# Performance work log

Measured on AMD Instinct MI355X. Metric: run time of the kernel, lower is better.

The kernel has to match this reference:

```python
import jax, jax.numpy as jnp
import numpy as np

PI = 3.1415926
NPERSEG, HOP = 512, 256
NFRAMES = 17
NFFT_BINS = 257
S = NFFT_BINS * NFRAMES  # 4369
NPATCH = 196
NFREQ = NPATCH // 2 + 1  # 99
D = 128
NF = 2
B = 32
TLEN = 4096

# periodic hann window (scipy default for spectral analysis)
_win_np = (0.5 - 0.5 * np.cos(2.0 * np.pi * np.arange(NPERSEG) / NPERSEG)).astype(np.float32)
WIN = jnp.asarray(_win_np)
WSUM = float(_win_np.sum())  # = 256
_idx_np = np.arange(NFRAMES)[:, None] * HOP + np.arange(NPERSEG)[None, :]
IDX = jnp.asarray(_idx_np)
IDX_FLAT = jnp.asarray(_idx_np.reshape(-1))
OLA_LEN = NPERSEG + (NFRAMES - 1) * HOP  # 4608


def _stft(x):
    # x: (B, D, T) real -> (B, D, 257, 17) complex; matches scipy.signal.stft
    # (window='hann', nperseg=512, noverlap=256, boundary='zeros', 'spectrum' scaling)
    xp = jnp.pad(x, ((0, 0), (0, 0), (HOP, HOP)))
    segs = xp[:, :, IDX] * WIN  # (B, D, 17, 512)
    Z = jnp.fft.rfft(segs, axis=-1) / WSUM
    return jnp.swapaxes(Z, -1, -2)


def _istft(Z):
    # Z: (B, D, 257, 17) complex -> (B, D, 4096) real; matches scipy.signal.istft
    b, d = Z.shape[0], Z.shape[1]
    frames = jnp.fft.irfft(Z, n=NPERSEG, axis=2) * WSUM * WIN[:, None]  # (B, D, 512, 17)
    frames = jnp.swapaxes(frames, 2, 3).reshape(b, d, NFRAMES * NPERSEG)
    ola = jnp.zeros((b, d, OLA_LEN), frames.dtype).at[:, :, IDX_FLAT].add(frames)
    norm = jnp.zeros((OLA_LEN,), frames.dtype).at[IDX_FLAT].add(jnp.tile(WIN * WIN, NFRAMES))
    return (ola / jnp.where(norm > 1e-10, norm, 1.0))[:, :, HOP:-HOP]


def _cx(p):
    return p[..., 0] + 1j * p[..., 1]


def _filter_bank(x, length, fb):
    # x * x / length summed against filter bank with dct-like cosine coefficients
    c = jnp.cos((2.0 * jnp.arange(1, NF + 1, dtype=jnp.float32) - 1.0) * PI / 2.0 * NF)
    fb_eff = jnp.sum(_cx(fb) * c[:, None, None], axis=0)
    return (x * x / length) * fb_eff


def _ln(x, g, b):
    m = x.mean(-1, keepdims=True)
    v = ((x - m) ** 2).mean(-1, keepdims=True)
    return (x - m) / jnp.sqrt(v + 1e-5) * g + b


def _addnorm(x, g1, b1, w1, bb1, w2, bb2, g2, b2):
    x = _ln(x, g1, b1)
    h = jax.nn.gelu(x @ w1 + bb1, approximate=False) @ w2 + bb2 + x
    return _ln(h, g2, b2)


def setup_inputs():
    key = jax.random.key(0)
    ks = jax.random.split(key, 12)
    sc = 0.05
    d = {}
    d["ecg"] = jax.random.normal(ks[0], (B, TLEN, D), jnp.float32)
    d["image"] = jax.random.normal(ks[1], (B, NPATCH, D), jnp.float32)
    d["tfb"] = jax.random.normal(ks[2], (NF, S, D, 2), jnp.float32)
    d["ifb"] = jax.random.normal(ks[3], (NF, NFREQ, D, 2), jnp.float32)
    d["i2t_sel"] = jax.random.normal(ks[4], (NFREQ, D, 2), jnp.float32)
    d["i2t_w"] = jax.random.normal(ks[5], (D, D), jnp.float32) * sc
    d["i2t_b"] = jnp.zeros((D,), jnp.float32)
    d["t_ln1_g"] = jnp.ones((D,), jnp.float32)
    d["t_ln1_b"] = jnp.zeros((D,), jnp.float32)
    d["t_w1"] = jax.random.normal(ks[6], (D, D), jnp.float32) * sc
    d["t_b1"] = jnp.zeros((D,), jnp.float32)
    d["t_w2"] = jax.random.normal(ks[7], (D, D), jnp.float32) * sc
    d["t_b2"] = jnp.zeros((D,), jnp.float32)
    d["t_ln2_g"] = jnp.ones((D,), jnp.float32)
    d["t_ln2_b"] = jnp.zeros((D,), jnp.float32)
    d["i_ln1_g"] = jnp.ones((D,), jnp.float32)
    d["i_ln1_b"] = jnp.zeros((D,), jnp.float32)
    d["i_w1"] = jax.random.normal(ks[8], (D, D), jnp.float32) * sc
    d["i_b1"] = jnp.zeros((D,), jnp.float32)
    d["i_w2"] = jax.random.normal(ks[9], (D, D), jnp.float32) * sc
    d["i_b2"] = jnp.zeros((D,), jnp.float32)
    d["i_ln2_g"] = jnp.ones((D,), jnp.float32)
    d["i_ln2_b"] = jnp.zeros((D,), jnp.float32)
    return d


def reference(ecg, image, tfb, ifb, i2t_sel, i2t_w, i2t_b,
              t_ln1_g, t_ln1_b, t_w1, t_b1, t_w2, t_b2, t_ln2_g, t_ln2_b,
              i_ln1_g, i_ln1_b, i_w1, i_b1, i_w2, i_b2, i_ln2_g, i_ln2_b):
    b, tlen, dm = ecg.shape
    n = image.shape[1]
    Z = _stft(jnp.swapaxes(ecg, 1, 2))  # (B, D, 257, 17)
    z_ecg = jnp.transpose(Z, (0, 2, 3, 1)).reshape(b, S, dm)  # (B, 4369, D) complex
    z_ecg = _filter_bank(z_ecg, S, tfb)
    z_img = jnp.fft.rfft(image, axis=1, norm="ortho")  # (B, 99, D)
    z_img = _filter_bank(z_img, NFREQ, ifb)
    # Image2TextGate: complex select, avg-pool real part over freq bins, 1x1 conv
    g = (z_img * _cx(i2t_sel)).real.mean(axis=1)  # (B, D)
    gate = (jnp.einsum("bd,ed->be", g, i2t_w) + i2t_b)[:, None, :]  # (B, 1, D)
    z_sel = z_ecg * gate
    ecg_t = _istft(jnp.transpose(z_sel.reshape(b, NFFT_BINS, NFRAMES, dm), (0, 3, 1, 2)))
    # torch detaches via numpy roundtrip -> stop_gradient
    ecg_t = jax.lax.stop_gradient(jnp.swapaxes(ecg_t, 1, 2))  # (B, T, D)
    text = _addnorm(ecg_t + ecg, t_ln1_g, t_ln1_b, t_w1, t_b1, t_w2, t_b2, t_ln2_g, t_ln2_b)
    # NOTE: original code discards image_frequency_select output and irffts the
    # filtered _image directly (bug preserved faithfully).
    img_t = jnp.fft.irfft(z_img, n=n, axis=1, norm="ortho")
    img_out = _addnorm(img_t + image, i_ln1_g, i_ln1_b, i_w1, i_b1, i_w2, i_b2, i_ln2_g, i_ln2_b)
    return (text, img_out)
```

## Files before the change

kernel.cpp:

```cpp
#include <hip/hip_runtime.h>
#include <math.h>

#define BB 32
#define DD 128
#define TLEN 4096
#define NSEG 512
#define HOP 256
#define NFR 17
#define NBINS 257
#define STOT 4369
#define NPATCH 196
#define NFREQ 99
#define OLAL 4608

#define FBT2_OFF 0
#define FBT2_SZ  (DD * NFR * NBINS * 2)
#define GBUF_OFF (FBT2_OFF + FBT2_SZ)
#define GATE_OFF (GBUF_OFF + BB * DD)
#define ZI_OFF   (GATE_OFF + BB * DD)
#define ZI_SZ    (BB * NFREQ * DD * 2)
#define X0I_OFF  (ZI_OFF + ZI_SZ)
#define X0I_SZ   (BB * NPATCH * DD)
#define XT_OFF   (X0I_OFF + X0I_SZ)
#define WF_OFF   (XT_OFF + BB * DD * TLEN)

typedef __attribute__((ext_vector_type(8))) short bf16x8;
typedef __attribute__((ext_vector_type(4))) float f32x4;
typedef __attribute__((ext_vector_type(8))) unsigned short u16x8;

__device__ __forceinline__ float gelu_exact(float x) {
    return 0.5f * x * (1.0f + erff(x * 0.70710678118654752f));
}

__device__ __forceinline__ short bf16_rne(float v) {
    unsigned b = __float_as_uint(v);
    return (short)((b + 0x7fffu + ((b >> 16) & 1u)) >> 16);
}

__device__ __forceinline__ void split8(float4 a, float4 b, bf16x8& hi, bf16x8& lo) {
    float v[8] = {a.x, a.y, a.z, a.w, b.x, b.y, b.z, b.w};
#pragma unroll
    for (int e = 0; e < 8; ++e) {
        unsigned bv = __float_as_uint(v[e]);
        unsigned hb = (bv + 0x7fffu + ((bv >> 16) & 1u)) & 0xffff0000u;
        float hf = __uint_as_float(hb);
        hi[e] = (short)(hb >> 16);
        lo[e] = bf16_rne(v[e] - hf);
    }
}

__global__ __launch_bounds__(256) void prep_wfrag(
    const float* __restrict__ w0, const float* __restrict__ w1,
    const float* __restrict__ w2, const float* __restrict__ w3,
    unsigned short* __restrict__ outw) {
    int id = blockIdx.x * 256 + threadIdx.x;
    if (id >= 4 * 2048) return;
    int m = id >> 11;
    int r = id & 2047;
    int kt = r >> 9;
    int n = (r >> 6) & 7;
    int lane = r & 63;
    int k0 = kt * 32 + (lane >> 4) * 8;
    int col = n * 16 + (lane & 15);
    const float* w = (m == 0) ? w0 : (m == 1) ? w1 : (m == 2) ? w2 : w3;
    u16x8 hi, lo;
#pragma unroll
    for (int e = 0; e < 8; ++e) {
        float v = w[(size_t)(k0 + e) * DD + col];
        unsigned bv = __float_as_uint(v);
        unsigned hb = (bv + 0x7fffu + ((bv >> 16) & 1u)) & 0xffff0000u;
        float hf = __uint_as_float(hb);
        float lres = v - hf;
        unsigned bl = __float_as_uint(lres);
        hi[e] = (unsigned short)(hb >> 16);
        lo[e] = (unsigned short)((bl + 0x7fffu + ((bl >> 16) & 1u)) >> 16);
    }
    u16x8* base = (u16x8*)(outw + (size_t)m * 32768);
    base[r] = hi;
    base[2048 + r] = lo;
}

__global__ __launch_bounds__(256) void prep_fb(const float* __restrict__ tfb,
                                               float* __restrict__ fbt2,
                                               float* __restrict__ gbuf) {
    int idx = blockIdx.x * 256 + threadIdx.x;
    if (idx < BB * DD) gbuf[idx] = 0.0f;
    if (idx >= STOT * DD) return;
    int d = idx & 127;
    int s = idx >> 7;
    float2 a = ((const float2*)tfb)[s * DD + d];
    float2 b = ((const float2*)tfb)[STOT * DD + s * DD + d];
    int f = s / NFR, t = s % NFR;
    float2 r;
    r.x = -(a.x + b.x);
    r.y = -(a.y + b.y);
    ((float2*)fbt2)[((size_t)d * NFR + t) * NBINS + f] = r;
}

__global__ __launch_bounds__(256) void transpose_btd(const float* __restrict__ in,
                                                     float* __restrict__ out) {
    __shared__ float tile[32][33];
    int b = blockIdx.z;
    int t0 = blockIdx.x * 32;
    int d0 = blockIdx.y * 32;
    int lx = threadIdx.x;
    int ly = threadIdx.y;
    for (int i = ly; i < 32; i += 8)
        tile[i][lx] = in[((size_t)b * TLEN + t0 + i) * DD + d0 + lx];
    __syncthreads();
    for (int i = ly; i < 32; i += 8)
        out[((size_t)b * DD + d0 + i) * TLEN + t0 + lx] = tile[lx][i];
}

__global__ __launch_bounds__(128) void img_dft(const float* __restrict__ image,
                                               const float* __restrict__ ifb,
                                               const float* __restrict__ sel,
                                               float* __restrict__ zi,
                                               float* __restrict__ gbuf) {
    __shared__ float ctab[NPATCH], stab[NPATCH];
    int b = blockIdx.x / 11;
    int fg = blockIdx.x % 11;
    int d = threadIdx.x;
    for (int m = d; m < NPATCH; m += 128) {
        ctab[m] = cospif(m * (2.0f / 196.0f));
        stab[m] = sinpif(m * (2.0f / 196.0f));
    }
    __syncthreads();
    float accr[9], acci[9];
    int mc[9];
#pragma unroll
    for (int j = 0; j < 9; ++j) { accr[j] = 0.0f; acci[j] = 0.0f; mc[j] = 0; }
    const float* img = image + (size_t)b * NPATCH * DD + d;
    for (int n = 0; n < NPATCH; ++n) {
        float v = img[(size_t)n * DD];
#pragma unroll
        for (int j = 0; j < 9; ++j) {
            float c = ctab[mc[j]], s = stab[mc[j]];
            accr[j] += v * c;
            acci[j] -= v * s;
            mc[j] += fg * 9 + j;
            if (mc[j] >= NPATCH) mc[j] -= NPATCH;
        }
    }
    float gg = 0.0f;
#pragma unroll
    for (int j = 0; j < 9; ++j) {
        int f = fg * 9 + j;
        float Xr = accr[j] * (1.0f / 14.0f);
        float Xi = acci[j] * (1.0f / 14.0f);
        float sr = (Xr * Xr - Xi * Xi) * (1.0f / 99.0f);
        float si = 2.0f * Xr * Xi * (1.0f / 99.0f);
        float2 f0 = ((const float2*)ifb)[f * DD + d];
        float2 f1 = ((const float2*)ifb)[NFREQ * DD + f * DD + d];
        float fbr = -(f0.x + f1.x), fbi = -(f0.y + f1.y);
        float zr = sr * fbr - si * fbi;
        float zm = sr * fbi + si * fbr;
        float2 o; o.x = zr; o.y = zm;
        ((float2*)zi)[((size_t)b * NFREQ + f) * DD + d] = o;
        float2 sl = ((const float2*)sel)[f * DD + d];
        gg += zr * sl.x - zm * sl.y;
    }
    atomicAdd(gbuf + b * DD + d, gg * (1.0f / 99.0f));
}

__global__ __launch_bounds__(128) void gate_kernel(const float* __restrict__ gbuf,
                                                   const float* __restrict__ w,
                                                   const float* __restrict__ bias,
                                                   float* __restrict__ gate) {
    __shared__ float gs[DD];
    int b = blockIdx.x, e = threadIdx.x;
    gs[e] = gbuf[b * DD + e];
    __syncthreads();
    float acc = bias[e];
    const float* wr = w + (size_t)e * DD;
    for (int d = 0; d < DD; ++d) acc += gs[d] * wr[d];
    gate[b * DD + e] = acc;
}

#define SWZ(e) ((e) ^ (((e) >> 4) & 15))

#define CMULW(dr, di, c, s, xr, xi) { float _t = (dr)*(c) - (di)*(s); xi = (dr)*(s) + (di)*(c); xr = _t; }
#define BF(xr, xi, h) { \
    float pr_ = __shfl_xor(xr, h), pi_ = __shfl_xor(xi, h); \
    float dr2_ = fmaf(sg##h, xr, pr_), di2_ = fmaf(sg##h, xi, pi_); \
    CMULW(dr2_, di2_, tc##h, ts##h, xr, xi) }
#define SSTG(h) BF(a0r, a0i, h) BF(a1r, a1i, h) BF(a2r, a2i, h) BF(a3r, a3i, h)
#define BF1(xr, xi) { \
    float pr_ = __shfl_xor(xr, 1), pi_ = __shfl_xor(xi, 1); \
    xr = fmaf(sg1, xr, pr_); xi = fmaf(sg1, xi, pi_); }
#define DIF256() { \
    float dr_, di_; \
    dr_ = a0r - a2r; di_ = a0i - a2i; a0r += a2r; a0i += a2i; CMULW(dr_, di_, wa_c, wa_s, a2r, a2i) \
    dr_ = a1r - a3r; di_ = a1i - a3i; a1r += a3r; a1i += a3i; CMULW(dr_, di_, wb_c, wb_s, a3r, a3i) \
    dr_ = a0r - a1r; di_ = a0i - a1i; a0r += a1r; a0i += a1i; CMULW(dr_, di_, wc_c, wc_s, a1r, a1i) \
    dr_ = a2r - a3r; di_ = a2i - a3i; a2r += a3r; a2i += a3i; CMULW(dr_, di_, wc_c, wc_s, a3r, a3i) \
    SSTG(32) SSTG(16) SSTG(8) SSTG(4) SSTG(2) \
    BF1(a0r, a0i) BF1(a1r, a1i) BF1(a2r, a2i) BF1(a3r, a3i) }

__global__ __launch_bounds__(256, 4) void stft_filter_istft(
    float* xT, const float* __restrict__ fbt2, const float* __restrict__ gate) {
    __shared__ float2 spec[NFR * 256];
    __shared__ float win[NSEG];
    __shared__ float rnorm[256];
    __shared__ float mct[129], mst[129];
    int tid = threadIdx.x;
    int lane = tid & 63, wave = tid >> 6;
    int bd = blockIdx.x;
    int d = bd & 127;
    float gat = gate[bd];
    const float scl = gat * (1.0f / 4369.0f);
    float* xrow = xT + (size_t)bd * TLEN;
    const float2* fbrow = (const float2*)(fbt2 + (size_t)d * NFR * NBINS * 2);

    for (int j = tid; j < NSEG; j += 256)
        win[j] = 0.5f - 0.5f * cospif(j * (1.0f / 256.0f));
    {
        float s2 = 0.5f - 0.5f * cospif(tid * (1.0f / 256.0f));
        float c2 = 1.0f - s2;
        rnorm[tid] = 1.0f / (s2 * s2 + c2 * c2);
    }
    if (tid < 129) {
        mct[tid] = cospif(tid * (1.0f / 256.0f));
        mst[tid] = sinpif(tid * (1.0f / 256.0f));
    }

    float wa_c = cospif(lane * (1.0f / 128.0f)), wa_s = -sinpif(lane * (1.0f / 128.0f));
    float wb_c = cospif((64 + lane) * (1.0f / 128.0f)), wb_s = -sinpif((64 + lane) * (1.0f / 128.0f));
    float wc_c = cospif(lane * (1.0f / 64.0f)),  wc_s = -sinpif(lane * (1.0f / 64.0f));
#define MKT(h) \
    float tc##h, ts##h, sg##h; \
    { int set_ = lane & h; float ang_ = (float)(lane & (h - 1)) * (1.0f / h); \
      tc##h = set_ ? cospif(ang_) : 1.0f; \
      ts##h = set_ ? -sinpif(ang_) : 0.0f; \
      sg##h = set_ ? -1.0f : 1.0f; }
    MKT(32) MKT(16) MKT(8) MKT(4) MKT(2)
    float sg1 = (lane & 1) ? -1.0f : 1.0f;
#undef MKT

    int eS[4], eL[4];
#pragma unroll
    for (int j = 0; j < 4; ++j) {
        int i = j * 64 + lane;
        eS[j] = SWZ((int)(__brev((unsigned)i) >> 24));
        eL[j] = SWZ(i);
    }
    __syncthreads();

    for (int t = wave; t < NFR; t += 4) {
        float a0r, a0i, a1r, a1i, a2r, a2i, a3r, a3i;
#define LOADJ(j, xr, xi) { \
        int i_ = (j) * 64 + lane; \
        int src_ = t * HOP + 2 * i_ - HOP; \
        float er_ = 0.0f, oi_ = 0.0f; \
        if (src_ >= 0 && src_ < TLEN) { \
            float2 v_ = *(const float2*)(xrow + src_); er_ = v_.x; oi_ = v_.y; } \
        float2 w_ = *(const float2*)(win + 2 * i_); \
        xr = er_ * w_.x; xi = oi_ * w_.y; }
        LOADJ(0, a0r, a0i) LOADJ(1, a1r, a1i) LOADJ(2, a2r, a2i) LOADJ(3, a3r, a3i)
#undef LOADJ
        DIF256()
        float2* sp = spec + t * 256;
        sp[eS[0]] = make_float2(a0r, a0i);
        sp[eS[1]] = make_float2(a1r, a1i);
        sp[eS[2]] = make_float2(a2r, a2i);
        sp[eS[3]] = make_float2(a3r, a3i);
    }
    __syncthreads();

    for (int j = tid; j < NFR * 129; j += 256) {
        int t = j / 129, m = j - t * 129;
        float2* sp = spec + t * 256;
        const float2* fbr = fbrow + t * NBINS;
        if (m == 0) {
            float2 v = sp[0];
            float re = v.x, im = v.y;
            float z0 = (re + im) * (1.0f / 256.0f);
            float zN = (re - im) * (1.0f / 256.0f);
            float2 fb0 = fbr[0], fbN = fbr[256];
            float y1r = z0 * z0 * fb0.x * scl;
            float y2r = zN * zN * fbN.x * scl;
            float Er = 0.5f * (y1r + y2r);
            float Dr = 0.5f * (y1r - y2r);
            sp[0] = make_float2(Er, -Dr);
        } else if (m == 128) {
            float2 v = sp[SWZ(128)];
            float Zr = v.x, Zi = v.y;
            float zr = Zr * (1.0f / 256.0f), zi2 = -Zi * (1.0f / 256.0f);
            float sr = zr * zr - zi2 * zi2, si = 2.0f * zr * zi2;
            float2 fb = fbr[128];
            sp[SWZ(128)] = make_float2((sr * fb.x - si * fb.y) * scl,
                                       (sr * fb.y + si * fb.x) * scl);
        } else {
            float2 vm = sp[SWZ(m)];
            float2 vc = sp[SWZ(256 - m)];
            float Amr = vm.x, Ami = vm.y;
            float Acr = vc.x, Aci = vc.y;
            float c = mct[m];
            float sn = mst[m];
            float y1r, y1i, y2r, y2i;
            {
                float Br = Acr, Bi = -Aci;
                float xer = 0.5f * (Amr + Br), xei = 0.5f * (Ami + Bi);
                float xo_r = 0.5f * (Ami - Bi), xo_i = -0.5f * (Amr - Br);
                float Xr = xer + c * xo_r + sn * xo_i;
                float Xi = xei + c * xo_i - sn * xo_r;
                float zr = Xr * (1.0f / 256.0f), zi2 = Xi * (1.0f / 256.0f);
                float sr = zr * zr - zi2 * zi2, si = 2.0f * zr * zi2;
                float2 fb = fbr[m];
                y1r = (sr * fb.x - si * fb.y) * scl;
                y1i = (sr * fb.y + si * fb.x) * scl;
            }
            {
                float Br = Amr, Bi = -Ami;
                float xer = 0.5f * (Acr + Br), xei = 0.5f * (Aci + Bi);
                float xo_r = 0.5f * (Aci - Bi), xo_i = -0.5f * (Acr - Br);
                float Xr = xer - c * xo_r + sn * xo_i;
                float Xi = xei - c * xo_i - sn * xo_r;
                float zr = Xr * (1.0f / 256.0f), zi2 = Xi * (1.0f / 256.0f);
                float sr = zr * zr - zi2 * zi2, si = 2.0f * zr * zi2;
                float2 fb = fbr[256 - m];
                y2r = (sr * fb.x - si * fb.y) * scl;
                y2i = (sr * fb.y + si * fb.x) * scl;
            }
            float Er = 0.5f * (y1r + y2r);
            float Ei = 0.5f * (y1i - y2i);
            float Dr = 0.5f * (y1r - y2r);
            float Di = 0.5f * (y1i + y2i);
            float Or = Dr * c - Di * sn;
            float Oi = Dr * sn + Di * c;
            sp[SWZ(m)] = make_float2(Er - Oi, -(Ei + Or));
            sp[SWZ(256 - m)] = make_float2(Er + Oi, Ei - Or);
        }
    }
    __syncthreads();

    for (int t = wave; t < NFR; t += 4) {
        float2* sp = spec + t * 256;
        float2 v0 = sp[eL[0]], v1 = sp[eL[1]], v2 = sp[eL[2]], v3 = sp[eL[3]];
        float a0r = v0.x, a0i = v0.y, a1r = v1.x, a1i = v1.y;
        float a2r = v2.x, a2i = v2.y, a3r = v3.x, a3i = v3.y;
        DIF256()
        sp[eS[0]] = make_float2(a0r, a0i);
        sp[eS[1]] = make_float2(a1r, a1i);
        sp[eS[2]] = make_float2(a2r, a2i);
        sp[eS[3]] = make_float2(a3r, a3i);
    }
    __syncthreads();

    const float* specf = (const float*)spec;
    for (int j = tid; j < TLEN; j += 256) {
        int p = j + HOP;
        int t1 = p >> 8, t0 = t1 - 1;
        int i1 = p & 255, i0 = i1 + 256;
        int comp = j & 1;
        float v1 = specf[(t1 * 256 + SWZ(i1 >> 1)) * 2 + comp];
        float v0 = specf[(t0 * 256 + SWZ(i0 >> 1)) * 2 + comp];
        if (comp) { v1 = -v1; v0 = -v0; }
        float s = v0 * win[i0] + v1 * win[i1];
        xrow[j] = s * rnorm[i1];
    }
}

__global__ __launch_bounds__(128) void img_irfft(const float* __restrict__ zi,
                                                 const float* __restrict__ image,
                                                 float* __restrict__ x0img) {
    __shared__ float ctab[NPATCH], stab[NPATCH];
    int b = blockIdx.x / 14;
    int ng = blockIdx.x % 14;
    int d = threadIdx.x;
    for (int m = d; m < NPATCH; m += 128) {
        ctab[m] = cospif(m * (2.0f / 196.0f));
        stab[m] = sinpif(m * (2.0f / 196.0f));
    }
    __syncthreads();
    const float2* zrow = (const float2*)zi + (size_t)b * NFREQ * DD + d;
    float acc[14];
    int mc[14];
    float2 z0 = zrow[0];
#pragma unroll
    for (int j = 0; j < 14; ++j) { acc[j] = z0.x; mc[j] = 0; }
    for (int f = 1; f <= 97; ++f) {
        float2 z = zrow[(size_t)f * DD];
#pragma unroll
        for (int j = 0; j < 14; ++j) {
            int n = ng * 14 + j;
            mc[j] += n;
            if (mc[j] >= NPATCH) mc[j] -= NPATCH;
            acc[j] += 2.0f * (z.x * ctab[mc[j]] - z.y * stab[mc[j]]);
        }
    }
    float2 z98 = zrow[98 * (size_t)DD];
#pragma unroll
    for (int j = 0; j < 14; ++j) {
        int n = ng * 14 + j;
        float a = acc[j] + ((n & 1) ? -z98.x : z98.x);
        float y = a * (1.0f / 14.0f);
        size_t idx = ((size_t)b * NPATCH + n) * DD + d;
        x0img[idx] = y + image[idx];
    }
}

#define XLNS 132

__device__ __forceinline__ void mlp_gemm(const float* __restrict__ ax,
                                         const unsigned short* __restrict__ wf,
                                         int lane, f32x4 acc[8]) {
#pragma unroll
    for (int n = 0; n < 8; ++n) acc[n] = (f32x4){0.f, 0.f, 0.f, 0.f};
    const bf16x8* bh0 = (const bf16x8*)wf;
    const bf16x8* bl0 = (const bf16x8*)(wf + 16384);
#pragma unroll 1
    for (int kt = 0; kt < 4; ++kt) {
        float4 va = *(const float4*)(ax + kt * 32);
        float4 vb = *(const float4*)(ax + kt * 32 + 4);
        bf16x8 ahi, alo;
        split8(va, vb, ahi, alo);
        const bf16x8* bh = bh0 + kt * 512 + lane;
        const bf16x8* bl = bl0 + kt * 512 + lane;
#pragma unroll
        for (int n = 0; n < 8; ++n) {
            bf16x8 wh = bh[n * 64];
            bf16x8 wl = bl[n * 64];
            acc[n] = __builtin_amdgcn_mfma_f32_16x16x32_bf16(ahi, wh, acc[n], 0, 0, 0);
            acc[n] = __builtin_amdgcn_mfma_f32_16x16x32_bf16(alo, wh, acc[n], 0, 0, 0);
            acc[n] = __builtin_amdgcn_mfma_f32_16x16x32_bf16(ahi, wl, acc[n], 0, 0, 0);
        }
    }
}

template <int FUSED>
__global__ __launch_bounds__(256) void addnorm_kernel(
    const float* __restrict__ srcA, const float* __restrict__ srcB,
    const float* __restrict__ ln1g, const float* __restrict__ ln1b,
    const unsigned short* __restrict__ w1f, const float* __restrict__ b1,
    const unsigned short* __restrict__ w2f, const float* __restrict__ b2,
    const float* __restrict__ ln2g, const float* __restrict__ ln2b,
    float* __restrict__ out) {
    __shared__ __align__(16) float xln[64 * XLNS];
    int tid = threadIdx.x;
    int b = 0, t0 = 0;
    size_t R0 = 0;
    if (FUSED) {
        b = blockIdx.x >> 6;
        t0 = (blockIdx.x & 63) * 64;
        for (int i = tid; i < 64 * 128; i += 256) {
            int dd = i >> 6, r = i & 63;
            xln[r * XLNS + dd] = srcA[((size_t)b * DD + dd) * TLEN + t0 + r];
        }
        __syncthreads();
        for (int i = tid; i < 64 * 128; i += 256) {
            int r = i >> 7, dd = i & 127;
            xln[r * XLNS + dd] += srcB[((size_t)b * TLEN + t0 + r) * DD + dd];
        }
    } else {
        R0 = (size_t)blockIdx.x * 64;
        for (int i = tid; i < 64 * 128; i += 256) {
            int r = i >> 7, dd = i & 127;
            xln[r * XLNS + dd] = srcA[(R0 + r) * DD + dd];
        }
    }
    __syncthreads();
    int wave = tid >> 6, lane = tid & 63;
    for (int r = wave; r < 64; r += 4) {
        float v0 = xln[r * XLNS + lane];
        float v1 = xln[r * XLNS + 64 + lane];
        float s = v0 + v1, ss = v0 * v0 + v1 * v1;
        for (int off = 32; off > 0; off >>= 1) {
            s += __shfl_xor(s, off);
            ss += __shfl_xor(ss, off);
        }
        float mean = s * (1.0f / 128.0f);
        float var = ss * (1.0f / 128.0f) - mean * mean;
        float rstd = rsqrtf(var + 1e-5f);
        xln[r * XLNS + lane] = (v0 - mean) * rstd * ln1g[lane] + ln1b[lane];
        xln[r * XLNS + 64 + lane] = (v1 - mean) * rstd * ln1g[64 + lane] + ln1b[64 + lane];
    }
    __syncthreads();
    int q = lane >> 4, c = lane & 15;
    int rbase = wave * 16 + q * 4;
    const float* ax = &xln[(wave * 16 + c) * XLNS + q * 8];
    f32x4 acc[8];
    mlp_gemm(ax, w1f, lane, acc);
    float res[8][4];
#pragma unroll
    for (int n = 0; n < 8; ++n)
#pragma unroll
        for (int r = 0; r < 4; ++r)
            res[n][r] = xln[(rbase + r) * XLNS + n * 16 + c];
#pragma unroll
    for (int n = 0; n < 8; ++n) {
        float bb = b1[n * 16 + c];
#pragma unroll
        for (int r = 0; r < 4; ++r)
            acc[n][r] = gelu_exact(acc[n][r] + bb);
    }
    __syncthreads();
#pragma unroll
    for (int n = 0; n < 8; ++n)
#pragma unroll
        for (int r = 0; r < 4; ++r)
            xln[(rbase + r) * XLNS + n * 16 + c] = acc[n][r];
    __syncthreads();
    mlp_gemm(ax, w2f, lane, acc);
#pragma unroll
    for (int n = 0; n < 8; ++n) {
        float bb = b2[n * 16 + c];
#pragma unroll
        for (int r = 0; r < 4; ++r)
            acc[n][r] += bb + res[n][r];
    }
    float s4[4] = {0.f, 0.f, 0.f, 0.f}, ss4[4] = {0.f, 0.f, 0.f, 0.f};
#pragma unroll
    for (int n = 0; n < 8; ++n)
#pragma unroll
        for (int r = 0; r < 4; ++r) {
            float h = acc[n][r];
            s4[r] += h; ss4[r] += h * h;
        }
#pragma unroll
    for (int off = 8; off > 0; off >>= 1) {
#pragma unroll
        for (int r = 0; r < 4; ++r) {
            s4[r] += __shfl_xor(s4[r], off);
            ss4[r] += __shfl_xor(ss4[r], off);
        }
    }
    float g2v[8], b2v[8];
#pragma unroll
    for (int n = 0; n < 8; ++n) {
        g2v[n] = ln2g[n * 16 + c];
        b2v[n] = ln2b[n * 16 + c];
    }
#pragma unroll
    for (int r = 0; r < 4; ++r) {
        float mean = s4[r] * (1.0f / 128.0f);
        float var = ss4[r] * (1.0f / 128.0f) - mean * mean;
        float rstd = rsqrtf(var + 1e-5f);
        size_t orow = FUSED ? ((size_t)b * TLEN + t0 + rbase + r) * DD
                            : (R0 + rbase + r) * DD;
#pragma unroll
        for (int n = 0; n < 8; ++n)
            out[orow + n * 16 + c] = (acc[n][r] - mean) * rstd * g2v[n] + b2v[n];
    }
}

extern "C" void kernel_launch(void* const* d_in, const int* in_sizes, int n_in,
                              void* d_out, int out_size, void* d_ws, size_t ws_size,
                              hipStream_t stream) {
    (void)in_sizes; (void)n_in; (void)out_size; (void)ws_size;
    const float* ecg   = (const float*)d_in[0];
    const float* image = (const float*)d_in[1];
    const float* tfb   = (const float*)d_in[2];
    const float* ifb   = (const float*)d_in[3];
    const float* sel   = (const float*)d_in[4];
    const float* i2t_w = (const float*)d_in[5];
    const float* i2t_b = (const float*)d_in[6];
    const float* t_ln1_g = (const float*)d_in[7];
    const float* t_ln1_b = (const float*)d_in[8];
    const float* t_w1 = (const float*)d_in[9];
    const float* t_b1 = (const float*)d_in[10];
    const float* t_w2 = (const float*)d_in[11];
    const float* t_b2 = (const float*)d_in[12];
    const float* t_ln2_g = (const float*)d_in[13];
    const float* t_ln2_b = (const float*)d_in[14];
    const float* i_ln1_g = (const float*)d_in[15];
    const float* i_ln1_b = (const float*)d_in[16];
    const float* i_w1 = (const float*)d_in[17];
    const float* i_b1 = (const float*)d_in[18];
    const float* i_w2 = (const float*)d_in[19];
    const float* i_b2 = (const float*)d_in[20];
    const float* i_ln2_g = (const float*)d_in[21];
    const float* i_ln2_b = (const float*)d_in[22];
    float* out = (float*)d_out;
    float* ws = (float*)d_ws;
    unsigned short* wfb = (unsigned short*)(ws + WF_OFF);

    prep_wfrag<<<32, 256, 0, stream>>>(t_w1, t_w2, i_w1, i_w2, wfb);
    prep_fb<<<(STOT * DD + 255) / 256, 256, 0, stream>>>(tfb, ws + FBT2_OFF, ws + GBUF_OFF);
    {
        dim3 tb(32, 8);
        dim3 tg(TLEN / 32, DD / 32, BB);
        transpose_btd<<<tg, tb, 0, stream>>>(ecg, ws + XT_OFF);
    }
    img_dft<<<BB * 11, 128, 0, stream>>>(image, ifb, sel, ws + ZI_OFF, ws + GBUF_OFF);
    gate_kernel<<<BB, 128, 0, stream>>>(ws + GBUF_OFF, i2t_w, i2t_b, ws + GATE_OFF);
    stft_filter_istft<<<BB * DD, 256, 0, stream>>>(ws + XT_OFF, ws + FBT2_OFF, ws + GATE_OFF);
    addnorm_kernel<1><<<BB * (TLEN / 64), 256, 0, stream>>>(
        ws + XT_OFF, ecg, t_ln1_g, t_ln1_b, wfb + 0, t_b1, wfb + 32768, t_b2,
        t_ln2_g, t_ln2_b, out);
    img_irfft<<<BB * 14, 128, 0, stream>>>(ws + ZI_OFF, image, ws + X0I_OFF);
    addnorm_kernel<0><<<(BB * NPATCH) / 64, 256, 0, stream>>>(
        ws + X0I_OFF, nullptr, i_ln1_g, i_ln1_b, wfb + 65536, i_b1, wfb + 98304, i_b2,
        i_ln2_g, i_ln2_b, out + (size_t)BB * TLEN * DD);
}
```

Measured before the change: 591.2 us.

## Merge prep kernels and overlap image irfft with text addnorm launch

Combines the weight-fragment prep, filter-bank transpose, ECG transpose and image DFT into one block-range-dispatched kernel. The image irfft is folded into the same launch as the text add-norm. The image gate reduction now writes per-group partial sums that gate_kernel adds up, replacing the atomics and the buffer zeroing. In the text add-norm, the residual ECG add moves into the LayerNorm pass, removing one shared-memory pass and a barrier. The aim is fewer launches and less tail idle time, at the cost of heterogeneous blocks sharing one launch configuration.

```diff
diff --git a/kernel.cpp b/kernel.cpp
--- a/kernel.cpp
+++ b/kernel.cpp
@@ -49,127 +49,144 @@
     }
 }
 
-__global__ __launch_bounds__(256) void prep_wfrag(
-    const float* __restrict__ w0, const float* __restrict__ w1,
-    const float* __restrict__ w2, const float* __restrict__ w3,
-    unsigned short* __restrict__ outw) {
-    int id = blockIdx.x * 256 + threadIdx.x;
-    if (id >= 4 * 2048) return;
-    int m = id >> 11;
-    int r = id & 2047;
-    int kt = r >> 9;
-    int n = (r >> 6) & 7;
-    int lane = r & 63;
-    int k0 = kt * 32 + (lane >> 4) * 8;
-    int col = n * 16 + (lane & 15);
-    const float* w = (m == 0) ? w0 : (m == 1) ? w1 : (m == 2) ? w2 : w3;
-    u16x8 hi, lo;
-#pragma unroll
-    for (int e = 0; e < 8; ++e) {
-        float v = w[(size_t)(k0 + e) * DD + col];
-        unsigned bv = __float_as_uint(v);
-        unsigned hb = (bv + 0x7fffu + ((bv >> 16) & 1u)) & 0xffff0000u;
-        float hf = __uint_as_float(hb);
-        float lres = v - hf;
-        unsigned bl = __float_as_uint(lres);
-        hi[e] = (unsigned short)(hb >> 16);
-        lo[e] = (unsigned short)((bl + 0x7fffu + ((bl >> 16) & 1u)) >> 16);
-    }
-    u16x8* base = (u16x8*)(outw + (size_t)m * 32768);
-    base[r] = hi;
-    base[2048 + r] = lo;
-}
-
-__global__ __launch_bounds__(256) void prep_fb(const float* __restrict__ tfb,
-                                               float* __restrict__ fbt2,
-                                               float* __restrict__ gbuf) {
-    int idx = blockIdx.x * 256 + threadIdx.x;
-    if (idx < BB * DD) gbuf[idx] = 0.0f;
-    if (idx >= STOT * DD) return;
-    int d = idx & 127;
-    int s = idx >> 7;
-    float2 a = ((const float2*)tfb)[s * DD + d];
-    float2 b = ((const float2*)tfb)[STOT * DD + s * DD + d];
-    int f = s / NFR, t = s % NFR;
-    float2 r;
-    r.x = -(a.x + b.x);
-    r.y = -(a.y + b.y);
-    ((float2*)fbt2)[((size_t)d * NFR + t) * NBINS + f] = r;
-}
-
-__global__ __launch_bounds__(256) void transpose_btd(const float* __restrict__ in,
-                                                     float* __restrict__ out) {
-    __shared__ float tile[32][33];
-    int b = blockIdx.z;
-    int t0 = blockIdx.x * 32;
-    int d0 = blockIdx.y * 32;
-    int lx = threadIdx.x;
-    int ly = threadIdx.y;
-    for (int i = ly; i < 32; i += 8)
-        tile[i][lx] = in[((size_t)b * TLEN + t0 + i) * DD + d0 + lx];
-    __syncthreads();
-    for (int i = ly; i < 32; i += 8)
-        out[((size_t)b * DD + d0 + i) * TLEN + t0 + lx] = tile[lx][i];
-}
-
-__global__ __launch_bounds__(128) void img_dft(const float* __restrict__ image,
-                                               const float* __restrict__ ifb,
-                                               const float* __restrict__ sel,
-                                               float* __restrict__ zi,
-                                               float* __restrict__ gbuf) {
-    __shared__ float ctab[NPATCH], stab[NPATCH];
-    int b = blockIdx.x / 11;
-    int fg = blockIdx.x % 11;
-    int d = threadIdx.x;
-    for (int m = d; m < NPATCH; m += 128) {
-        ctab[m] = cospif(m * (2.0f / 196.0f));
-        stab[m] = sinpif(m * (2.0f / 196.0f));
-    }
-    __syncthreads();
-    float accr[9], acci[9];
-    int mc[9];
-#pragma unroll
-    for (int j = 0; j < 9; ++j) { accr[j] = 0.0f; acci[j] = 0.0f; mc[j] = 0; }
-    const float* img = image + (size_t)b * NPATCH * DD + d;
-    for (int n = 0; n < NPATCH; ++n) {
-        float v = img[(size_t)n * DD];
-#pragma unroll
-        for (int j = 0; j < 9; ++j) {
-            float c = ctab[mc[j]], s = stab[mc[j]];
-            accr[j] += v * c;
-            acci[j] -= v * s;
-            mc[j] += fg * 9 + j;
-            if (mc[j] >= NPATCH) mc[j] -= NPATCH;
-        }
-    }
-    float gg = 0.0f;
-#pragma unroll
-    for (int j = 0; j < 9; ++j) {
-        int f = fg * 9 + j;
-        float Xr = accr[j] * (1.0f / 14.0f);
-        float Xi = acci[j] * (1.0f / 14.0f);
-        float sr = (Xr * Xr - Xi * Xi) * (1.0f / 99.0f);
-        float si = 2.0f * Xr * Xi * (1.0f / 99.0f);
-        float2 f0 = ((const float2*)ifb)[f * DD + d];
-        float2 f1 = ((const float2*)ifb)[NFREQ * DD + f * DD + d];
-        float fbr = -(f0.x + f1.x), fbi = -(f0.y + f1.y);
-        float zr = sr * fbr - si * fbi;
-        float zm = sr * fbi + si * fbr;
-        float2 o; o.x = zr; o.y = zm;
-        ((float2*)zi)[((size_t)b * NFREQ + f) * DD + d] = o;
-        float2 sl = ((const float2*)sel)[f * DD + d];
-        gg += zr * sl.x - zm * sl.y;
-    }
-    atomicAdd(gbuf + b * DD + d, gg * (1.0f / 99.0f));
-}
-
-__global__ __launch_bounds__(128) void gate_kernel(const float* __restrict__ gbuf,
+#define PA_DFT0   0
+#define PA_DFTN   (BB * 11)
+#define PA_WF0    (PA_DFT0 + PA_DFTN)
+#define PA_WFN    32
+#define PA_FB0    (PA_WF0 + PA_WFN)
+#define PA_FBN    ((STOT * DD + 255) / 256)
+#define PA_TR0    (PA_FB0 + PA_FBN)
+#define PA_TRN    ((TLEN / 32) * (DD / 32) * BB)
+#define PA_TOT    (PA_TR0 + PA_TRN)
+
+__global__ __launch_bounds__(256) void prep_all(
+    const float* __restrict__ tw1, const float* __restrict__ tw2,
+    const float* __restrict__ iw1, const float* __restrict__ iw2,
+    unsigned short* __restrict__ outw,
+    const float* __restrict__ tfb, float* __restrict__ fbt2,
+    const float* __restrict__ ecg, float* __restrict__ xT,
+    const float* __restrict__ image, const float* __restrict__ ifb,
+    const float* __restrict__ sel, float* __restrict__ zi,
+    float* __restrict__ gpart) {
+    __shared__ float smem[32 * 33];
+    int bid = blockIdx.x;
+    int tid = threadIdx.x;
+
+    if (bid < PA_DFTN) {
+        float* ctab = smem;
+        float* stab = smem + 200;
+        int b = bid / 11;
+        int fg = bid % 11;
+        for (int m = tid; m < NPATCH; m += 256) {
+            ctab[m] = cospif(m * (2.0f / 196.0f));
+            stab[m] = sinpif(m * (2.0f / 196.0f));
+        }
+        __syncthreads();
+        if (tid < 128) {
+            int d = tid;
+            float accr[9], acci[9];
+            int mc[9];
+#pragma unroll
+            for (int j = 0; j < 9; ++j) { accr[j] = 0.0f; acci[j] = 0.0f; mc[j] = 0; }
+            const float* img = image + (size_t)b * NPATCH * DD + d;
+            for (int n = 0; n < NPATCH; ++n) {
+                float v = img[(size_t)n * DD];
+#pragma unroll
+                for (int j = 0; j < 9; ++j) {
+                    float c = ctab[mc[j]], s = stab[mc[j]];
+                    accr[j] += v * c;
+                    acci[j] -= v * s;
+                    mc[j] += fg * 9 + j;
+                    if (mc[j] >= NPATCH) mc[j] -= NPATCH;
+                }
+            }
+            float gg = 0.0f;
+#pragma unroll
+            for (int j = 0; j < 9; ++j) {
+                int f = fg * 9 + j;
+                float Xr = accr[j] * (1.0f / 14.0f);
+                float Xi = acci[j] * (1.0f / 14.0f);
+                float sr = (Xr * Xr - Xi * Xi) * (1.0f / 99.0f);
+                float si = 2.0f * Xr * Xi * (1.0f / 99.0f);
+                float2 f0 = ((const float2*)ifb)[f * DD + d];
+                float2 f1 = ((const float2*)ifb)[NFREQ * DD + f * DD + d];
+                float fbr = -(f0.x + f1.x), fbi = -(f0.y + f1.y);
+                float zr = sr * fbr - si * fbi;
+                float zm = sr * fbi + si * fbr;
+                float2 o; o.x = zr; o.y = zm;
+                ((float2*)zi)[((size_t)b * NFREQ + f) * DD + d] = o;
+                float2 sl = ((const float2*)sel)[f * DD + d];
+                gg += zr * sl.x - zm * sl.y;
+            }
+            gpart[((size_t)fg * BB + b) * DD + d] = gg * (1.0f / 99.0f);
+        }
+    } else if (bid < PA_FB0) {
+        int id = (bid - PA_WF0) * 256 + tid;
+        if (id < 4 * 2048) {
+            int m = id >> 11;
+            int r = id & 2047;
+            int kt = r >> 9;
+            int n = (r >> 6) & 7;
+            int lane = r & 63;
+            int k0 = kt * 32 + (lane >> 4) * 8;
+            int col = n * 16 + (lane & 15);
+            const float* w = (m == 0) ? tw1 : (m == 1) ? tw2 : (m == 2) ? iw1 : iw2;
+            u16x8 hi, lo;
+#pragma unroll
+            for (int e = 0; e < 8; ++e) {
+                float v = w[(size_t)(k0 + e) * DD + col];
+                unsigned bv = __float_as_uint(v);
+                unsigned hb = (bv + 0x7fffu + ((bv >> 16) & 1u)) & 0xffff0000u;
+                float hf = __uint_as_float(hb);
+                float lres = v - hf;
+                unsigned bl = __float_as_uint(lres);
+                hi[e] = (unsigned short)(hb >> 16);
+                lo[e] = (unsigned short)((bl + 0x7fffu + ((bl >> 16) & 1u)) >> 16);
+            }
+            u16x8* base = (u16x8*)(outw + (size_t)m * 32768);
+            base[r] = hi;
+            base[2048 + r] = lo;
+        }
+    } else if (bid < PA_TR0) {
+        int idx = (bid - PA_FB0) * 256 + tid;
+        if (idx < STOT * DD) {
+            int d = idx & 127;
+            int s = idx >> 7;
+            float2 a = ((const float2*)tfb)[s * DD + d];
+            float2 b2 = ((const float2*)tfb)[STOT * DD + s * DD + d];
+            int f = s / NFR, t = s % NFR;
+            float2 r;
+            r.x = -(a.x + b2.x);
+            r.y = -(a.y + b2.y);
+            ((float2*)fbt2)[((size_t)d * NFR + t) * NBINS + f] = r;
+        }
+    } else {
+        int rel = bid - PA_TR0;
+        int t0 = (rel & 127) * 32;
+        int d0 = ((rel >> 7) & 3) * 32;
+        int b = rel >> 9;
+        int lx = tid & 31;
+        int ly = tid >> 5;
+        float (*tile)[33] = (float (*)[33])smem;
+        for (int i = ly; i < 32; i += 8)
+            tile[i][lx] = ecg[((size_t)b * TLEN + t0 + i) * DD + d0 + lx];
+        __syncthreads();
+        for (int i = ly; i < 32; i += 8)
+            xT[((size_t)b * DD + d0 + i) * TLEN + t0 + lx] = tile[lx][i];
+    }
+}
+
+__global__ __launch_bounds__(128) void gate_kernel(const float* __restrict__ gpart,
                                                    const float* __restrict__ w,
                                                    const float* __restrict__ bias,
                                                    float* __restrict__ gate) {
     __shared__ float gs[DD];
     int b = blockIdx.x, e = threadIdx.x;
-    gs[e] = gbuf[b * DD + e];
+    float acc0 = 0.0f;
+#pragma unroll
+    for (int fg = 0; fg < 11; ++fg)
+        acc0 += gpart[((size_t)fg * BB + b) * DD + e];
+    gs[e] = acc0;
     __syncthreads();
     float acc = bias[e];
     const float* wr = w + (size_t)e * DD;
@@ -361,45 +378,6 @@
     }
 }
 
-__global__ __launch_bounds__(128) void img_irfft(const float* __restrict__ zi,
-                                                 const float* __restrict__ image,
-                                                 float* __restrict__ x0img) {
-    __shared__ float ctab[NPATCH], stab[NPATCH];
-    int b = blockIdx.x / 14;
-    int ng = blockIdx.x % 14;
-    int d = threadIdx.x;
-    for (int m = d; m < NPATCH; m += 128) {
-        ctab[m] = cospif(m * (2.0f / 196.0f));
-        stab[m] = sinpif(m * (2.0f / 196.0f));
-    }
-    __syncthreads();
-    const float2* zrow = (const float2*)zi + (size_t)b * NFREQ * DD + d;
-    float acc[14];
-    int mc[14];
-    float2 z0 = zrow[0];
-#pragma unroll
-    for (int j = 0; j < 14; ++j) { acc[j] = z0.x; mc[j] = 0; }
-    for (int f = 1; f <= 97; ++f) {
-        float2 z = zrow[(size_t)f * DD];
-#pragma unroll
-        for (int j = 0; j < 14; ++j) {
-            int n = ng * 14 + j;
-            mc[j] += n;
-            if (mc[j] >= NPATCH) mc[j] -= NPATCH;
-            acc[j] += 2.0f * (z.x * ctab[mc[j]] - z.y * stab[mc[j]]);
-        }
-    }
-    float2 z98 = zrow[98 * (size_t)DD];
-#pragma unroll
-    for (int j = 0; j < 14; ++j) {
-        int n = ng * 14 + j;
-        float a = acc[j] + ((n & 1) ? -z98.x : z98.x);
-        float y = a * (1.0f / 14.0f);
-        size_t idx = ((size_t)b * NPATCH + n) * DD + d;
-        x0img[idx] = y + image[idx];
-    }
-}
-
 #define XLNS 132
 
 __device__ __forceinline__ void mlp_gemm(const float* __restrict__ ax,
@@ -429,31 +407,26 @@
 }
 
 template <int FUSED>
-__global__ __launch_bounds__(256) void addnorm_kernel(
+__device__ __forceinline__ void addnorm_body(
+    int bid, float* xln,
     const float* __restrict__ srcA, const float* __restrict__ srcB,
     const float* __restrict__ ln1g, const float* __restrict__ ln1b,
     const unsigned short* __restrict__ w1f, const float* __restrict__ b1,
     const unsigned short* __restrict__ w2f, const float* __restrict__ b2,
     const float* __restrict__ ln2g, const float* __restrict__ ln2b,
     float* __restrict__ out) {
-    __shared__ __align__(16) float xln[64 * XLNS];
     int tid = threadIdx.x;
     int b = 0, t0 = 0;
     size_t R0 = 0;
     if (FUSED) {
-        b = blockIdx.x >> 6;
-        t0 = (blockIdx.x & 63) * 64;
+        b = bid >> 6;
+        t0 = (bid & 63) * 64;
         for (int i = tid; i < 64 * 128; i += 256) {
             int dd = i >> 6, r = i & 63;
             xln[r * XLNS + dd] = srcA[((size_t)b * DD + dd) * TLEN + t0 + r];
         }
-        __syncthreads();
-        for (int i = tid; i < 64 * 128; i += 256) {
-            int r = i >> 7, dd = i & 127;
-            xln[r * XLNS + dd] += srcB[((size_t)b * TLEN + t0 + r) * DD + dd];
-        }
     } else {
-        R0 = (size_t)blockIdx.x * 64;
+        R0 = (size_t)bid * 64;
         for (int i = tid; i < 64 * 128; i += 256) {
             int r = i >> 7, dd = i & 127;
             xln[r * XLNS + dd] = srcA[(R0 + r) * DD + dd];
@@ -461,9 +434,14 @@
     }
     __syncthreads();
     int wave = tid >> 6, lane = tid & 63;
+    const float* pB = FUSED ? srcB + ((size_t)b * TLEN + t0) * DD : nullptr;
     for (int r = wave; r < 64; r += 4) {
         float v0 = xln[r * XLNS + lane];
         float v1 = xln[r * XLNS + 64 + lane];
+        if (FUSED) {
+            v0 += pB[(size_t)r * DD + lane];
+            v1 += pB[(size_t)r * DD + 64 + lane];
+        }
         float s = v0 + v1, ss = v0 * v0 + v1 * v1;
         for (int off = 32; off > 0; off >>= 1) {
             s += __shfl_xor(s, off);
@@ -542,6 +520,78 @@
         for (int n = 0; n < 8; ++n)
             out[orow + n * 16 + c] = (acc[n][r] - mean) * rstd * g2v[n] + b2v[n];
     }
+}
+
+#define F2_AN  (BB * (TLEN / 64))
+#define F2_IR  (BB * 14)
+
+__global__ __launch_bounds__(256) void fused_text_img(
+    const float* __restrict__ srcA, const float* __restrict__ ecg,
+    const float* __restrict__ ln1g, const float* __restrict__ ln1b,
+    const unsigned short* __restrict__ w1f, const float* __restrict__ b1,
+    const unsigned short* __restrict__ w2f, const float* __restrict__ b2,
+    const float* __restrict__ ln2g, const float* __restrict__ ln2b,
+    float* __restrict__ out,
+    const float* __restrict__ zi, const float* __restrict__ image,
+    float* __restrict__ x0img) {
+    __shared__ __align__(16) float xln[64 * XLNS];
+    int bid = blockIdx.x;
+    int tid = threadIdx.x;
+    if (bid < F2_AN) {
+        addnorm_body<1>(bid, xln, srcA, ecg, ln1g, ln1b, w1f, b1, w2f, b2,
+                        ln2g, ln2b, out);
+    } else {
+        int rel = bid - F2_AN;
+        float* ctab = xln;
+        float* stab = xln + 200;
+        int b = rel / 14;
+        int ng = rel % 14;
+        for (int m = tid; m < NPATCH; m += 256) {
+            ctab[m] = cospif(m * (2.0f / 196.0f));
+            stab[m] = sinpif(m * (2.0f / 196.0f));
+        }
+        __syncthreads();
+        if (tid < 128) {
+            int d = tid;
+            const float2* zrow = (const float2*)zi + (size_t)b * NFREQ * DD + d;
+            float acc[14];
+            int mc[14];
+            float2 z0 = zrow[0];
+#pragma unroll
+            for (int j = 0; j < 14; ++j) { acc[j] = z0.x; mc[j] = 0; }
+            for (int f = 1; f <= 97; ++f) {
+                float2 z = zrow[(size_t)f * DD];
+#pragma unroll
+                for (int j = 0; j < 14; ++j) {
+                    int n = ng * 14 + j;
+                    mc[j] += n;
+                    if (mc[j] >= NPATCH) mc[j] -= NPATCH;
+                    acc[j] += 2.0f * (z.x * ctab[mc[j]] - z.y * stab[mc[j]]);
+                }
+            }
+            float2 z98 = zrow[98 * (size_t)DD];
+#pragma unroll
+            for (int j = 0; j < 14; ++j) {
+                int n = ng * 14 + j;
+                float a = acc[j] + ((n & 1) ? -z98.x : z98.x);
+                float y = a * (1.0f / 14.0f);
+                size_t idx = ((size_t)b * NPATCH + n) * DD + d;
+                x0img[idx] = y + image[idx];
+            }
+        }
+    }
+}
+
+__global__ __launch_bounds__(256) void addnorm_img(
+    const float* __restrict__ srcA,
+    const float* __restrict__ ln1g, const float* __restrict__ ln1b,
+    const unsigned short* __restrict__ w1f, const float* __restrict__ b1,
+    const unsigned short* __restrict__ w2f, const float* __restrict__ b2,
+    const float* __restrict__ ln2g, const float* __restrict__ ln2b,
+    float* __restrict__ out) {
+    __shared__ __align__(16) float xln[64 * XLNS];
+    addnorm_body<0>(blockIdx.x, xln, srcA, nullptr, ln1g, ln1b, w1f, b1,
+                    w2f, b2, ln2g, ln2b, out);
 }
 
 extern "C" void kernel_launch(void* const* d_in, const int* in_sizes, int n_in,
@@ -574,22 +624,20 @@
     float* out = (float*)d_out;
     float* ws = (float*)d_ws;
     unsigned short* wfb = (unsigned short*)(ws + WF_OFF);
-
-    prep_wfrag<<<32, 256, 0, stream>>>(t_w1, t_w2, i_w1, i_w2, wfb);
-    prep_fb<<<(STOT * DD + 255) / 256, 256, 0, stream>>>(tfb, ws + FBT2_OFF, ws + GBUF_OFF);
-    {
-        dim3 tb(32, 8);
-        dim3 tg(TLEN / 32, DD / 32, BB);
-        transpose_btd<<<tg, tb, 0, stream>>>(ecg, ws + XT_OFF);
-    }
-    img_dft<<<BB * 11, 128, 0, stream>>>(image, ifb, sel, ws + ZI_OFF, ws + GBUF_OFF);
-    gate_kernel<<<BB, 128, 0, stream>>>(ws + GBUF_OFF, i2t_w, i2t_b, ws + GATE_OFF);
+    float* gpart = ws + X0I_OFF;
+
+    prep_all<<<PA_TOT, 256, 0, stream>>>(
+        t_w1, t_w2, i_w1, i_w2, wfb,
+        tfb, ws + FBT2_OFF,
+        ecg, ws + XT_OFF,
+        image, ifb, sel, ws + ZI_OFF, gpart);
+    gate_kernel<<<BB, 128, 0, stream>>>(gpart, i2t_w, i2t_b, ws + GATE_OFF);
     stft_filter_istft<<<BB * DD, 256, 0, stream>>>(ws + XT_OFF, ws + FBT2_OFF, ws + GATE_OFF);
-    addnorm_kernel<1><<<BB * (TLEN / 64), 256, 0, stream>>>(
+    fused_text_img<<<F2_AN + F2_IR, 256, 0, stream>>>(
         ws + XT_OFF, ecg, t_ln1_g, t_ln1_b, wfb + 0, t_b1, wfb + 32768, t_b2,
-        t_ln2_g, t_ln2_b, out);
-    img_irfft<<<BB * 14, 128, 0, stream>>>(ws + ZI_OFF, image, ws + X0I_OFF);
-    addnorm_kernel<0><<<(BB * NPATCH) / 64, 256, 0, stream>>>(
-        ws + X0I_OFF, nullptr, i_ln1_g, i_ln1_b, wfb + 65536, i_b1, wfb + 98304, i_b2,
+        t_ln2_g, t_ln2_b, out,
+        ws + ZI_OFF, image, ws + X0I_OFF);
+    addnorm_img<<<(BB * NPATCH) / 64, 256, 0, stream>>>(
+        ws + X0I_OFF, i_ln1_g, i_ln1_b, wfb + 65536, i_b1, wfb + 98304, i_b2,
         i_ln2_g, i_ln2_b, out + (size_t)BB * TLEN * DD);
 }
```

Result: faster. 570.0 us (-3.6%).
